# Performance work log

Measured on AMD Instinct MI355X. Metric: run time of the kernel, lower is better.

## Reference

```python
import jax, jax.numpy as jnp
import numpy as np

B, D, C = 4096, 768, 80
PRIV = np.arange(0, 20)        # privileged label indices
NONPRIV = np.arange(20, 80)    # non-privileged label indices
EPS = 1e-8
BETA = 1.0
EPSILON = 0.1
DIMS = [768, 256, 64, 16, 4, 1]


def setup_inputs() -> dict:
    key = jax.random.key(0)
    ks = jax.random.split(key, 12)
    inp = {
        "hidden": jax.random.normal(ks[0], (B, D), dtype=jnp.float32),
        "labels": jax.random.randint(ks[1], (B, C), 0, 2, dtype=jnp.int32),
    }
    ki = 2
    for wpref, bpref in (("W", "b"), ("rW", "rb")):
        for i in range(5):
            din, dout = DIMS[i], DIMS[i + 1]
            inp[f"{wpref}{i+1}"] = (jax.random.normal(ks[ki], (C, din, dout), dtype=jnp.float32)
                                     * (1.0 / np.sqrt(din)))
            inp[f"{bpref}{i+1}"] = jnp.zeros((C, dout), dtype=jnp.float32)
            ki += 1
    return inp


def _scores(hidden, Ws, bs):
    # c independent MLP heads applied to the same hidden state, batched over c.
    x = jnp.einsum('bd,cdh->bch', hidden, Ws[0]) + bs[0]  # (b, c, 256)
    for W, b in zip(Ws[1:], bs[1:]):
        x = jnp.einsum('bch,cho->bco', jax.nn.relu(x), W) + b
    return jax.nn.sigmoid(x[..., 0])  # (b, c)


def _bce(p, y):
    p = jnp.clip(p, EPS, 1.0 - EPS)
    return -(y * jnp.log(p) + (1.0 - y) * jnp.log1p(-p))


def _losses(scores, ref_scores, labels):
    ref_scores = jax.lax.stop_gradient(ref_scores)  # ref head is frozen
    # --- privileged pairwise margin loss (vectorized masked form) ---
    log_term = jnp.log(scores / (ref_scores + EPS) + EPS)  # (b, c)
    ps = scores[:, PRIV]                                   # (b, P)
    pos = labels[:, PRIV] == 1                             # (b, P)
    neg = labels == 0                                      # (b, c)
    # confusing negative k for positive privileged l: y_k==0 and s_k >= s_l
    conf = pos[:, :, None] & neg[:, None, :] & (scores[:, None, :] >= ps[:, :, None])
    h_w = log_term[:, PRIV][:, :, None] - log_term[:, None, :]   # (b, P, c)
    pair_loss = -jax.nn.log_sigmoid(BETA * h_w)
    n_pairs = conf.sum()
    total = jnp.where(conf, pair_loss, 0.0).sum()
    loss_priv = jnp.where(n_pairs > 0, total / jnp.maximum(n_pairs, 1), 0.0)
    # --- non-privileged hinged BCE ---
    y = labels[:, NONPRIV].astype(jnp.float32)
    loss_cur = _bce(scores[:, NONPRIV], y)
    loss_ref = jax.lax.stop_gradient(_bce(ref_scores[:, NONPRIV], y))
    loss_nonpriv = jnp.mean(jax.nn.relu(loss_cur - loss_ref - EPSILON))
    return jnp.stack([loss_priv, loss_nonpriv])


def reference(hidden, labels, W1, b1, W2, b2, W3, b3, W4, b4, W5, b5,
              rW1, rb1, rW2, rb2, rW3, rb3, rW4, rb4, rW5, rb5):
    scores = _scores(hidden, (W1, W2, W3, W4, W5), (b1, b2, b3, b4, b5))
    ref_scores = _scores(hidden, (rW1, rW2, rW3, rW4, rW5), (rb1, rb2, rb3, rb4, rb5))
    return _losses(scores, ref_scores, labels)
```

## Files before the change

kernel.cpp:

```cpp
#include <hip/hip_runtime.h>
#include <math.h>

typedef __attribute__((ext_vector_type(8))) short short8;
typedef __attribute__((ext_vector_type(4))) float f32x4;

#define Bn   4096
#define Dn   768
#define Cn   80
#define H1   256
#define H2   64
#define H3   16
#define H4   4

__device__ inline ushort f2bf(float f) {
    union { float f; unsigned u; } v; v.f = f;
    unsigned r = v.u + 0x7fffu + ((v.u >> 16) & 1u);
    return (ushort)(r >> 16);
}
__device__ inline unsigned pack2(float a, float b) {
    return (unsigned)f2bf(a) | ((unsigned)f2bf(b) << 16);
}
__device__ inline void load_lds16(const void* g, void* l) {
    __builtin_amdgcn_global_load_lds(
        (const __attribute__((address_space(1))) void*)g,
        (__attribute__((address_space(3))) void*)l, 16, 0, 0);
}

#define FENCE() asm volatile("" ::: "memory")
#define BAR() do { FENCE(); __builtin_amdgcn_sched_barrier(0); \
                   __builtin_amdgcn_s_barrier(); \
                   __builtin_amdgcn_sched_barrier(0); FENCE(); } while (0)
#define VMCNT6() do { asm volatile("s_waitcnt vmcnt(6)" ::: "memory"); \
                      __builtin_amdgcn_sched_barrier(0); } while (0)
#define VMCNT0() do { asm volatile("s_waitcnt vmcnt(0)" ::: "memory"); \
                      __builtin_amdgcn_sched_barrier(0); } while (0)

__global__ __launch_bounds__(256)
void convert_all(const float* __restrict__ hidden, ushort* __restrict__ hbs,
                 const float* __restrict__ W1, const float* __restrict__ rW1,
                 ushort* __restrict__ dstW1,
                 const float* __restrict__ W2, const float* __restrict__ rW2,
                 const float* __restrict__ W3, const float* __restrict__ rW3,
                 ushort* __restrict__ dstW2, ushort* __restrict__ dstW3)
{
    __shared__ float l[32 * H1];
    const int t = threadIdx.x;
    const int b = blockIdx.x;

    if (b < 768) {
        const int kt = b % 24;
        const int bt = b / 24;
        char* out = (char*)hbs + ((size_t)bt * 24 + kt) * 8192;
        #pragma unroll
        for (int ch = 0; ch < 2; ++ch) {
            const int o = (ch * 256 + t) * 16;
            const int r = o >> 6;
            const int s = (o >> 4) & 3;
            const int k0 = (s ^ ((r >> 1) & 3)) * 8;
            const float* src = hidden + (size_t)(bt * 128 + r) * Dn + kt * 32 + k0;
            const float4 f0 = ((const float4*)src)[0];
            const float4 f1 = ((const float4*)src)[1];
            uint4 w;
            w.x = pack2(f0.x, f0.y); w.y = pack2(f0.z, f0.w);
            w.z = pack2(f1.x, f1.y); w.w = pack2(f1.z, f1.w);
            *(uint4*)(out + o) = w;
        }
    } else if (b < 4608) {
        const int i = b - 768;
        const int kt2 = i % 24;
        const int c   = (i / 24) % Cn;
        const int set = i / (24 * Cn);
        const float* src = (set ? rW1 : W1) + ((size_t)c * Dn + kt2 * 32) * H1;
        #pragma unroll
        for (int q = 0; q < 8; ++q)
            ((float4*)l)[q * 256 + t] = ((const float4*)src)[q * 256 + t];
        __syncthreads();
        char* out = (char*)dstW1 + (((size_t)set * Cn + c) * 24 + kt2) * 16384;
        #pragma unroll
        for (int rd = 0; rd < 4; ++rd) {
            const int o = (rd * 256 + t) * 16;
            const int n = o >> 6;
            const int s = (o >> 4) & 3;
            const int kk0 = (s ^ ((n >> 1) & 3)) * 8;
            uint4 w;
            w.x = pack2(l[(kk0 + 0) * H1 + n], l[(kk0 + 1) * H1 + n]);
            w.y = pack2(l[(kk0 + 2) * H1 + n], l[(kk0 + 3) * H1 + n]);
            w.z = pack2(l[(kk0 + 4) * H1 + n], l[(kk0 + 5) * H1 + n]);
            w.w = pack2(l[(kk0 + 6) * H1 + n], l[(kk0 + 7) * H1 + n]);
            *(uint4*)(out + o) = w;
        }
    } else {
        const int i = b - 4608;
        const int bx  = i % 5;
        const int c   = (i / 5) % Cn;
        const int set = i / (5 * Cn);
        if (bx < 4) {
            const float* src = (set ? rW2 : W2) + ((size_t)c * H1 + bx * 64) * H2;
            #pragma unroll
            for (int q = 0; q < 4; ++q)
                ((float4*)l)[q * 256 + t] = ((const float4*)src)[q * 256 + t];
            __syncthreads();
            char* out = (char*)dstW2 + (((size_t)set * Cn + c) * 4 + bx) * 8192;
            #pragma unroll
            for (int rd = 0; rd < 2; ++rd) {
                const int idx = rd * 256 + t;
                const int n = idx >> 3;
                const int s = idx & 7;
                const int o = n * 128 + ((s << 4) ^ ((n & 7) << 4));
                const int kk0 = s * 8;
                uint4 w;
                w.x = pack2(l[(kk0 + 0) * H2 + n], l[(kk0 + 1) * H2 + n]);
                w.y = pack2(l[(kk0 + 2) * H2 + n], l[(kk0 + 3) * H2 + n]);
                w.z = pack2(l[(kk0 + 4) * H2 + n], l[(kk0 + 5) * H2 + n]);
                w.w = pack2(l[(kk0 + 6) * H2 + n], l[(kk0 + 7) * H2 + n]);
                *(uint4*)(out + o) = w;
            }
        } else if (t < 128) {
            const float* src = (set ? rW3 : W3) + (size_t)c * (H2 * H3);
            char* out = (char*)dstW3 + ((size_t)set * Cn + c) * 2048;
            const int o = t * 16;
            const int n = o >> 7;
            const int slot = (o >> 4) & 7;
            const int kk0 = (slot ^ (n & 7)) * 8;
            uint4 w;
            w.x = pack2(src[(kk0 + 0) * H3 + n], src[(kk0 + 1) * H3 + n]);
            w.y = pack2(src[(kk0 + 2) * H3 + n], src[(kk0 + 3) * H3 + n]);
            w.z = pack2(src[(kk0 + 4) * H3 + n], src[(kk0 + 5) * H3 + n]);
            w.w = pack2(src[(kk0 + 6) * H3 + n], src[(kk0 + 7) * H3 + n]);
            *(uint4*)(out + o) = w;
        }
    }
}


__device__ __forceinline__ void stageA(char* lds, const char* hb, int slot, int kt, int t) {
    const char* g = hb + (size_t)kt * 8192 + t * 16;
    char* l = lds + slot * 8192 + t * 16;
    load_lds16(g,        l);
    load_lds16(g + 4096, l + 4096);
}
__device__ __forceinline__ void stageB(char* lds, const char* w1b, int slot, int kt, int t) {
    const char* g = w1b + (size_t)kt * 16384 + t * 16;
    char* l = lds + 24576 + slot * 16384 + t * 16;
    load_lds16(g,         l);
    load_lds16(g + 4096,  l + 4096);
    load_lds16(g + 8192,  l + 8192);
    load_lds16(g + 12288, l + 12288);
}

__global__ __launch_bounds__(256, 2)
void scores_mfma_w128(const ushort* __restrict__ hbs, const ushort* __restrict__ W1ts,
                      const ushort* __restrict__ W2ts, const ushort* __restrict__ W3ts,
                      const float* __restrict__ b1, const float* __restrict__ rb1,
                      const float* __restrict__ b2, const float* __restrict__ rb2,
                      const float* __restrict__ b3, const float* __restrict__ rb3,
                      const float* __restrict__ W4, const float* __restrict__ rW4,
                      const float* __restrict__ b4, const float* __restrict__ rb4,
                      const float* __restrict__ W5, const float* __restrict__ rW5,
                      const float* __restrict__ b5, const float* __restrict__ rb5,
                      float* __restrict__ scores)
{
    __shared__ uint4 smv[73728 / 16];
    char* lds = (char*)smv;

    const int t = threadIdx.x;
    const int wid = t >> 6, lane = t & 63;
    const int lrow = lane & 15;
    const int lkg  = lane >> 4;
    const int lk   = lkg * 8;
    const int wr  = wid >> 1;
    const int wcn = wid & 1;

    const int cpx = 5120 >> 3;
    const int wg  = (blockIdx.x & 7) * cpx + (blockIdx.x >> 3);
    const int set = wg / 2560;
    const int rem = wg % 2560;
    const int c   = rem / 32;
    const int bt  = rem % 32;

    const float* pb1 = set ? rb1 : b1;
    const float* pb2 = set ? rb2 : b2;
    const float* pb3 = set ? rb3 : b3;
    const float* pW4 = set ? rW4 : W4;  const float* pb4 = set ? rb4 : b4;
    const float* pW5 = set ? rW5 : W5;  const float* pb5 = set ? rb5 : b5;

    const char* hb  = (const char*)hbs + (size_t)bt * 196608;
    const char* w1b = (const char*)W1ts + (size_t)(set * Cn + c) * 393216;

    f32x4 acc[4][8];
    #pragma unroll
    for (int i = 0; i < 4; ++i)
        #pragma unroll
        for (int j = 0; j < 8; ++j)
            acc[i][j] = (f32x4){0.f, 0.f, 0.f, 0.f};

    stageA(lds, hb, 0, 0, t);  stageB(lds, w1b, 0, 0, t);
    stageA(lds, hb, 1, 1, t);  stageB(lds, w1b, 1, 1, t);
    VMCNT6();
    BAR();

    #pragma unroll 3
    for (int j = 0; j < 24; ++j) {
        const int rs = j % 3;
        short8 breg[8], areg[4];
        {
            const char* bb = lds + 24576 + rs * 16384;
            const char* ab = lds + rs * 8192;
            #pragma unroll
            for (int nt = 0; nt < 8; ++nt) {
                const int col = wcn * 128 + nt * 16 + lrow;
                breg[nt] = *(const short8*)(bb + col * 64
                              + ((2 * lk) ^ (((col >> 1) & 3) << 4)));
            }
            #pragma unroll
            for (int mt = 0; mt < 4; ++mt) {
                const int row = wr * 64 + mt * 16 + lrow;
                areg[mt] = *(const short8*)(ab + row * 64
                              + ((2 * lk) ^ (((row >> 1) & 3) << 4)));
            }
        }
        {
            const int ws = (j + 2) % 3;
            int ka = j + 2; if (ka >= 24) ka -= 24;
            stageA(lds, hb, ws, ka, t);
            stageB(lds, w1b, ws, ka, t);
        }
        VMCNT6();
        __builtin_amdgcn_s_setprio(1);
        #pragma unroll
        for (int mt = 0; mt < 4; ++mt)
            #pragma unroll
            for (int nt = 0; nt < 8; ++nt)
                acc[mt][nt] = __builtin_amdgcn_mfma_f32_16x16x32_bf16(
                    breg[nt], areg[mt], acc[mt][nt], 0, 0, 0);
        __builtin_amdgcn_s_setprio(0);
        BAR();
    }
    VMCNT0();
    BAR();

    {
        float4 bias1[8];
        #pragma unroll
        for (int nt = 0; nt < 8; ++nt)
            bias1[nt] = *(const float4*)&pb1[(size_t)c * H1 + wcn * 128 + nt * 16 + lkg * 4];
        #pragma unroll
        for (int mt = 0; mt < 4; ++mt) {
            const int row = wr * 64 + mt * 16 + lrow;
            const int swz = (row & 7) << 4;
            #pragma unroll
            for (int nt = 0; nt < 8; ++nt) {
                const float* bb = (const float*)&bias1[nt];
                uint2 w;
                w.x = pack2(fmaxf(acc[mt][nt][0] + bb[0], 0.f),
                            fmaxf(acc[mt][nt][1] + bb[1], 0.f));
                w.y = pack2(fmaxf(acc[mt][nt][2] + bb[2], 0.f),
                            fmaxf(acc[mt][nt][3] + bb[3], 0.f));
                const int off = row * 512 + ((wcn * 256 + nt * 32 + lkg * 8) ^ swz);
                *(uint2*)(lds + off) = w;
            }
        }
    }
    BAR();

    f32x4 acc2[2][4];
    #pragma unroll
    for (int i = 0; i < 2; ++i)
        #pragma unroll
        for (int j = 0; j < 4; ++j)
            acc2[i][j] = (f32x4){0.f, 0.f, 0.f, 0.f};
    {
        const char* w2b = (const char*)W2ts + (size_t)(set * Cn + c) * 32768;
        #pragma unroll
        for (int ksz = 0; ksz < 8; ++ksz) {
            short8 b2r[4], a2[2];
            const int kk2 = (ksz & 1) * 32 + lk;
            #pragma unroll
            for (int nt = 0; nt < 4; ++nt) {
                const int col = nt * 16 + lrow;
                b2r[nt] = *(const short8*)(w2b + (ksz >> 1) * 8192
                             + ((col * 128 + 2 * kk2) ^ ((col & 7) << 4)));
            }
            const int k = ksz * 32 + lk;
            #pragma unroll
            for (int m2 = 0; m2 < 2; ++m2) {
                const int row = wid * 32 + m2 * 16 + lrow;
                a2[m2] = *(const short8*)(lds + ((row * 512 + 2 * k) ^ ((row & 7) << 4)));
            }
            #pragma unroll
            for (int m2 = 0; m2 < 2; ++m2)
                #pragma unroll
                for (int nt = 0; nt < 4; ++nt)
                    acc2[m2][nt] = __builtin_amdgcn_mfma_f32_16x16x32_bf16(
                        b2r[nt], a2[m2], acc2[m2][nt], 0, 0, 0);
        }
    }
    BAR();

    {
        float4 bias2[4];
        #pragma unroll
        for (int nt = 0; nt < 4; ++nt)
            bias2[nt] = *(const float4*)&pb2[(size_t)c * H2 + nt * 16 + lkg * 4];
        #pragma unroll
        for (int m2 = 0; m2 < 2; ++m2) {
            const int row = wid * 32 + m2 * 16 + lrow;
            const int swz = (row & 7) << 4;
            #pragma unroll
            for (int nt = 0; nt < 4; ++nt) {
                const float* bb = (const float*)&bias2[nt];
                uint2 w;
                w.x = pack2(fmaxf(acc2[m2][nt][0] + bb[0], 0.f),
                            fmaxf(acc2[m2][nt][1] + bb[1], 0.f));
                w.y = pack2(fmaxf(acc2[m2][nt][2] + bb[2], 0.f),
                            fmaxf(acc2[m2][nt][3] + bb[3], 0.f));
                const int off = row * 128 + ((nt * 32 + lkg * 8) ^ swz);
                *(uint2*)(lds + off) = w;
            }
        }
    }
    BAR();

    {
        const char* w3t = (const char*)W3ts + (size_t)(set * Cn + c) * 2048;
        short8 w3f[2];
        #pragma unroll
        for (int ks = 0; ks < 2; ++ks)
            w3f[ks] = *(const short8*)(w3t + lrow * 128
                         + ((2 * (ks * 32 + lk)) ^ ((lrow & 7) << 4)));
        f32x4 acc3[2];
        #pragma unroll
        for (int m2 = 0; m2 < 2; ++m2) acc3[m2] = (f32x4){0.f, 0.f, 0.f, 0.f};
        #pragma unroll
        for (int m2 = 0; m2 < 2; ++m2) {
            const int row = wid * 32 + m2 * 16 + lrow;
            #pragma unroll
            for (int ks = 0; ks < 2; ++ks) {
                const short8 xf = *(const short8*)(lds + row * 128
                                     + ((2 * (ks * 32 + lk)) ^ ((row & 7) << 4)));
                acc3[m2] = __builtin_amdgcn_mfma_f32_16x16x32_bf16(
                    w3f[ks], xf, acc3[m2], 0, 0, 0);
            }
        }

        const float4 b3v = *(const float4*)&pb3[(size_t)c * H3 + lkg * 4];
        const float* w4c = pW4 + (size_t)c * (H3 * H4);
        float4 w4r[4];
        #pragma unroll
        for (int r = 0; r < 4; ++r)
            w4r[r] = *(const float4*)&w4c[(lkg * 4 + r) * H4];
        const float4 b4v = *(const float4*)&pb4[(size_t)c * H4];
        const float4 w5v = *(const float4*)&pW5[(size_t)c * H4];
        const float bb5 = pb5[c];

        #pragma unroll
        for (int m2 = 0; m2 < 2; ++m2) {
            float p4[4] = {0.f, 0.f, 0.f, 0.f};
            #pragma unroll
            for (int r = 0; r < 4; ++r) {
                const float x3 = fmaxf(acc3[m2][r] + ((const float*)&b3v)[r], 0.f);
                const float* wr4 = (const float*)&w4r[r];
                #pragma unroll
                for (int o = 0; o < 4; ++o)
                    p4[o] = fmaf(x3, wr4[o], p4[o]);
            }
            #pragma unroll
            for (int o = 0; o < 4; ++o) {
                p4[o] += __shfl_xor(p4[o], 16, 64);
                p4[o] += __shfl_xor(p4[o], 32, 64);
            }
            float x5 = bb5;
            #pragma unroll
            for (int o = 0; o < 4; ++o)
                x5 = fmaf(fmaxf(p4[o] + ((const float*)&b4v)[o], 0.f),
                          ((const float*)&w5v)[o], x5);
            const float sc = 1.f / (1.f + expf(-x5));
            if (lkg == 0)
                scores[((size_t)set * Bn + bt * 128 + wid * 32 + m2 * 16 + lrow) * Cn + c] = sc;
        }
    }
}

__device__ inline float bce_f(float p, float y) {
    p = fminf(fmaxf(p, 1e-8f), 1.0f - 1e-8f);
    return -(y * logf(p) + (1.f - y) * log1pf(-p));
}

__global__ __launch_bounds__(128)
void loss_kernel(const float* __restrict__ scores, const int* __restrict__ labels,
                 float* __restrict__ pair_sum, float* __restrict__ np_sum,
                 int* __restrict__ pair_cnt)
{
    __shared__ float ss[Cn], lt[Cn];
    __shared__ int lab[Cn];
    __shared__ float redf[128], redn[128];
    __shared__ int redi[128];

    const int b = blockIdx.x, t = threadIdx.x;
    float np_local = 0.f, ps_local = 0.f;
    int pc_local = 0;

    if (t < Cn) {
        const float s  = scores[(size_t)b * Cn + t];
        const float sr = scores[(size_t)Bn * Cn + (size_t)b * Cn + t];
        const int l = labels[(size_t)b * Cn + t];
        ss[t] = s; lab[t] = l;
        lt[t] = logf(s / (sr + 1e-8f) + 1e-8f);
        if (t >= 20) {
            const float y = (float)l;
            np_local = fmaxf(bce_f(s, y) - bce_f(sr, y) - 0.1f, 0.f);
        }
    }
    __syncthreads();
    if (t < Cn && lab[t] == 0) {
        const float sj = ss[t], ltj = lt[t];
        #pragma unroll
        for (int i = 0; i < 20; ++i) {
            if (lab[i] == 1 && sj >= ss[i]) {
                const float z = -(lt[i] - ltj);
                ps_local += fmaxf(z, 0.f) + log1pf(expf(-fabsf(z)));
                pc_local++;
            }
        }
    }
    redf[t] = ps_local; redn[t] = np_local; redi[t] = pc_local;
    __syncthreads();
    for (int s = 64; s > 0; s >>= 1) {
        if (t < s) { redf[t] += redf[t + s]; redn[t] += redn[t + s]; redi[t] += redi[t + s]; }
        __syncthreads();
    }
    if (t == 0) { pair_sum[b] = redf[0]; np_sum[b] = redn[0]; pair_cnt[b] = redi[0]; }
}

__global__ __launch_bounds__(1024)
void final_kernel(const float* __restrict__ pair_sum, const int* __restrict__ pair_cnt,
                  const float* __restrict__ np_sum, float* __restrict__ out)
{
    __shared__ float r1[1024], r2[1024];
    __shared__ int ri[1024];
    const int t = threadIdx.x;
    float s1 = 0.f, s2 = 0.f; int c1 = 0;
    for (int i = t; i < Bn; i += 1024) { s1 += pair_sum[i]; c1 += pair_cnt[i]; s2 += np_sum[i]; }
    r1[t] = s1; r2[t] = s2; ri[t] = c1;
    __syncthreads();
    for (int s = 512; s > 0; s >>= 1) {
        if (t < s) { r1[t] += r1[t + s]; r2[t] += r2[t + s]; ri[t] += ri[t + s]; }
        __syncthreads();
    }
    if (t == 0) {
        const int n = ri[0];
        out[0] = (n > 0) ? (r1[0] / (float)(n > 1 ? n : 1)) : 0.f;
        out[1] = r2[0] / (float)(Bn * 60);
    }
}

static inline size_t alup(size_t x) { return (x + 4095) & ~(size_t)4095; }

extern "C" void kernel_launch(void* const* d_in, const int* in_sizes, int n_in,
                              void* d_out, int out_size, void* d_ws, size_t ws_size,
                              hipStream_t stream)
{
    const float* hidden = (const float*)d_in[0];
    const int*   labels = (const int*)d_in[1];
    const float* W1 = (const float*)d_in[2];   const float* b1 = (const float*)d_in[3];
    const float* W2 = (const float*)d_in[4];   const float* b2 = (const float*)d_in[5];
    const float* W3 = (const float*)d_in[6];   const float* b3 = (const float*)d_in[7];
    const float* W4 = (const float*)d_in[8];   const float* b4 = (const float*)d_in[9];
    const float* W5 = (const float*)d_in[10];  const float* b5 = (const float*)d_in[11];
    const float* rW1 = (const float*)d_in[12]; const float* rb1 = (const float*)d_in[13];
    const float* rW2 = (const float*)d_in[14]; const float* rb2 = (const float*)d_in[15];
    const float* rW3 = (const float*)d_in[16]; const float* rb3 = (const float*)d_in[17];
    const float* rW4 = (const float*)d_in[18]; const float* rb4 = (const float*)d_in[19];
    const float* rW5 = (const float*)d_in[20]; const float* rb5 = (const float*)d_in[21];

    char* ws = (char*)d_ws;
    const size_t off_scores = 0;
    const size_t sz_scores  = (size_t)2 * Bn * Cn * 4;
    const size_t off_pair   = alup(off_scores + sz_scores);
    const size_t sz_pair    = (size_t)3 * Bn * 4;
    const size_t off_hbs    = alup(off_pair + sz_pair);
    const size_t sz_hbs     = (size_t)Bn * Dn * 2;
    const size_t off_w1t    = alup(off_hbs + sz_hbs);
    const size_t sz_w1t     = (size_t)2 * Cn * 24 * 16384;
    const size_t off_w2t    = alup(off_w1t + sz_w1t);
    const size_t sz_w2t     = (size_t)2 * Cn * 4 * 8192;
    const size_t off_w3t    = alup(off_w2t + sz_w2t);

    float* scoresb  = (float*)(ws + off_scores);
    float* pair_sum = (float*)(ws + off_pair);
    float* np_sum   = pair_sum + Bn;
    int*   pair_cnt = (int*)(np_sum + Bn);
    float* out      = (float*)d_out;

    ushort* hbs  = (ushort*)(ws + off_hbs);
    ushort* W1ts = (ushort*)(ws + off_w1t);
    ushort* W2ts = (ushort*)(ws + off_w2t);
    ushort* W3ts = (ushort*)(ws + off_w3t);

    convert_all<<<5408, 256, 0, stream>>>(hidden, hbs, W1, rW1, W1ts,
                                          W2, rW2, W3, rW3, W2ts, W3ts);

    scores_mfma_w128<<<5120, 256, 0, stream>>>(hbs, W1ts, W2ts, W3ts,
        b1, rb1, b2, rb2, b3, rb3, W4, rW4, b4, rb4, W5, rW5, b5, rb5,
        scoresb);
    loss_kernel<<<Bn, 128, 0, stream>>>(scoresb, labels, pair_sum, np_sum, pair_cnt);
    final_kernel<<<1, 1024, 0, stream>>>(pair_sum, pair_cnt, np_sum, out);
}
```

Before: 334.5 us.

## Double-buffer LDS fragments in registers to overlap LDS reads with MFMA

```diff
diff --git a/kernel.cpp b/kernel.cpp
--- a/kernel.cpp
+++ b/kernel.cpp
@@ -30,10 +30,15 @@
 #define BAR() do { FENCE(); __builtin_amdgcn_sched_barrier(0); \
                    __builtin_amdgcn_s_barrier(); \
                    __builtin_amdgcn_sched_barrier(0); FENCE(); } while (0)
-#define VMCNT6() do { asm volatile("s_waitcnt vmcnt(6)" ::: "memory"); \
+#define VMCNT6() do { __builtin_amdgcn_sched_barrier(0); \
+                      asm volatile("s_waitcnt vmcnt(6)" ::: "memory"); \
                       __builtin_amdgcn_sched_barrier(0); } while (0)
-#define VMCNT0() do { asm volatile("s_waitcnt vmcnt(0)" ::: "memory"); \
+#define VMCNT0() do { __builtin_amdgcn_sched_barrier(0); \
+                      asm volatile("s_waitcnt vmcnt(0)" ::: "memory"); \
                       __builtin_amdgcn_sched_barrier(0); } while (0)
+#define LGKM0() do { __builtin_amdgcn_sched_barrier(0); \
+                     asm volatile("s_waitcnt lgkmcnt(0)" ::: "memory"); \
+                     __builtin_amdgcn_sched_barrier(0); } while (0)
 
 __global__ __launch_bounds__(256)
 void convert_all(const float* __restrict__ hidden, ushort* __restrict__ hbs,
@@ -199,43 +204,63 @@
     VMCNT6();
     BAR();
 
+    short8 brC[8], arC[4], brN[8], arN[4];
+    {
+        const char* bb = lds + 24576;
+        const char* ab = lds;
+        #pragma unroll
+        for (int nt = 0; nt < 8; ++nt) {
+            const int col = wcn * 128 + nt * 16 + lrow;
+            brC[nt] = *(const short8*)(bb + col * 64 + ((2 * lk) ^ (((col >> 1) & 3) << 4)));
+        }
+        #pragma unroll
+        for (int mt = 0; mt < 4; ++mt) {
+            const int row = wr * 64 + mt * 16 + lrow;
+            arC[mt] = *(const short8*)(ab + row * 64 + ((2 * lk) ^ (((row >> 1) & 3) << 4)));
+        }
+    }
+
+    #define ITER_BODY(J, CURB, CURA, NXTB, NXTA) do {                          \
+        const int ws_ = ((J) + 2) % 3;                                         \
+        int ka_ = (J) + 2; if (ka_ >= 24) ka_ -= 24;      \
+        stageA(lds, hb, ws_, ka_, t);                                          \
+        stageB(lds, w1b, ws_, ka_, t);                                         \
+        VMCNT6();                                                              \
+        BAR();                                                                 \
+        { const int rs_ = ((J) + 1) % 3;                                       \
+          const char* bb_ = lds + 24576 + rs_ * 16384;                         \
+          const char* ab_ = lds + rs_ * 8192;                                  \
+          _Pragma("unroll")                                                    \
+          for (int nt = 0; nt < 8; ++nt) {                                     \
+              const int col_ = wcn * 128 + nt * 16 + lrow;                     \
+              NXTB[nt] = *(const short8*)(bb_ + col_ * 64                      \
+                            + ((2 * lk) ^ (((col_ >> 1) & 3) << 4)));          \
+          }                                                                    \
+          _Pragma("unroll")                                                    \
+          for (int mt = 0; mt < 4; ++mt) {                                     \
+              const int row_ = wr * 64 + mt * 16 + lrow;                       \
+              NXTA[mt] = *(const short8*)(ab_ + row_ * 64                      \
+                            + ((2 * lk) ^ (((row_ >> 1) & 3) << 4)));          \
+          } }                                                                  \
+        __builtin_amdgcn_s_setprio(1);                                         \
+        _Pragma("unroll")                                                      \
+        for (int mt = 0; mt < 4; ++mt)                                         \
+            _Pragma("unroll")                                                  \
+            for (int nt = 0; nt < 8; ++nt)                                     \
+                acc[mt][nt] = __builtin_amdgcn_mfma_f32_16x16x32_bf16(         \
+                    CURB[nt], CURA[mt], acc[mt][nt], 0, 0, 0);                 \
+        __builtin_amdgcn_s_setprio(0);                                         \
+        LGKM0();                                                               \
+    } while (0)
+
     #pragma unroll 3
-    for (int j = 0; j < 24; ++j) {
-        const int rs = j % 3;
-        short8 breg[8], areg[4];
-        {
-            const char* bb = lds + 24576 + rs * 16384;
-            const char* ab = lds + rs * 8192;
-            #pragma unroll
-            for (int nt = 0; nt < 8; ++nt) {
-                const int col = wcn * 128 + nt * 16 + lrow;
-                breg[nt] = *(const short8*)(bb + col * 64
-                              + ((2 * lk) ^ (((col >> 1) & 3) << 4)));
-            }
-            #pragma unroll
-            for (int mt = 0; mt < 4; ++mt) {
-                const int row = wr * 64 + mt * 16 + lrow;
-                areg[mt] = *(const short8*)(ab + row * 64
-                              + ((2 * lk) ^ (((row >> 1) & 3) << 4)));
-            }
-        }
-        {
-            const int ws = (j + 2) % 3;
-            int ka = j + 2; if (ka >= 24) ka -= 24;
-            stageA(lds, hb, ws, ka, t);
-            stageB(lds, w1b, ws, ka, t);
-        }
-        VMCNT6();
-        __builtin_amdgcn_s_setprio(1);
-        #pragma unroll
-        for (int mt = 0; mt < 4; ++mt)
-            #pragma unroll
-            for (int nt = 0; nt < 8; ++nt)
-                acc[mt][nt] = __builtin_amdgcn_mfma_f32_16x16x32_bf16(
-                    breg[nt], areg[mt], acc[mt][nt], 0, 0, 0);
-        __builtin_amdgcn_s_setprio(0);
-        BAR();
-    }
+    for (int jp = 0; jp < 12; ++jp) {
+        const int j0 = jp * 2;
+        ITER_BODY(j0,     brC, arC, brN, arN);
+        ITER_BODY(j0 + 1, brN, arN, brC, arC);
+    }
+    #undef ITER_BODY
+
     VMCNT0();
     BAR();
 
```

After: 349.9 us. 4.6% more time.
